# Kernel optimization log

Hardware: AMD Instinct MI355X
Metric: run time of the kernel (lower is better)

## Reference

```python
import jax, jax.numpy as jnp
import numpy as np

N, E, F, H, C, G = 100000, 1600000, 128, 128, 1, 512
NLAYERS, DT, ALPHA, GAMMA = 5, 1.0, 1.0, 1.0


def setup_inputs() -> dict:
    key = jax.random.key(0)
    ks = jax.random.split(key, 11)
    x = jax.random.normal(ks[0], (N, F), dtype=jnp.float32)
    edge_index = jax.random.randint(ks[1], (2, E), 0, N, dtype=jnp.int64)
    batch = jnp.sort(jax.random.randint(ks[2], (N,), 0, G, dtype=jnp.int64))
    s = 1.0 / np.sqrt(H).astype(np.float32)
    W_enc = jax.random.normal(ks[3], (H, F), jnp.float32) * (1.0 / np.sqrt(F))
    b_enc = jnp.zeros((H,), jnp.float32)
    W_conv = jax.random.normal(ks[4], (H, H), jnp.float32) * s
    b_conv = jnp.zeros((H,), jnp.float32)
    W_res = jax.random.normal(ks[5], (H, H), jnp.float32) * s
    b_res = jnp.zeros((H,), jnp.float32)
    W_dec = jax.random.normal(ks[6], (C, H), jnp.float32) * s
    b_dec = jnp.zeros((C,), jnp.float32)
    return {
        "x": x, "edge_index": edge_index, "batch": batch,
        "W_enc": W_enc, "b_enc": b_enc,
        "W_conv": W_conv, "b_conv": b_conv,
        "W_res": W_res, "b_res": b_res,
        "W_dec": W_dec, "b_dec": b_dec,
    }


def reference(x, edge_index, batch, W_enc, b_enc, W_conv, b_conv, W_res, b_res, W_dec, b_dec):
    src, dst = edge_index[0], edge_index[1]
    # GCN symmetric normalization with self-loops: deg = 1 + in-degree(dst)
    deg = jnp.zeros((N,), x.dtype).at[dst].add(1.0) + 1.0
    dinv = jax.lax.rsqrt(deg)
    norm = dinv[src] * dinv[dst]            # [E]
    self_norm = (dinv * dinv)[:, None]      # [N,1] self-loop coefficient

    def gcn_conv(X):
        xw = X @ W_conv.T                   # lin (bias=False)
        agg = jnp.zeros_like(xw).at[dst].add(norm[:, None] * xw[src])
        agg = agg + self_norm * xw          # self-loop term
        return agg + b_conv

    Y = x @ W_enc.T + b_enc
    Xs = Y
    for _ in range(NLAYERS):
        res = Xs @ W_res.T + b_res - Xs @ W_conv.T   # res(X) - conv.lin(X)
        Y = Y + DT * (jax.nn.relu(gcn_conv(Xs) + res) - ALPHA * Y - GAMMA * Xs)
        Xs = Xs + DT * Y
    out = Xs @ W_dec.T + b_dec               # [N, 1]
    pooled = jax.ops.segment_sum(out, batch, num_segments=G)  # [G, 1]
    return pooled.squeeze(-1)                # [G]
```

## Files before the change

### kernel.cpp

```cpp
#include <hip/hip_runtime.h>
#include <hip/hip_bf16.h>
#include <stdint.h>


#define HD 128
#define SCHUNK 2048

typedef __attribute__((ext_vector_type(4))) float f32x4;
typedef __attribute__((ext_vector_type(8))) float f32x8;
typedef __attribute__((ext_vector_type(8))) _Float16 f16x8;

__global__ __launch_bounds__(256) void k_deg(const int* __restrict__ dst, int E,
                                             int* __restrict__ cnt){
  int e = blockIdx.x * 256 + threadIdx.x;
  if (e < E) atomicAdd(&cnt[dst[e]], 1);
}

__global__ __launch_bounds__(256) void k_scan_part(const int* __restrict__ cnt,
                                                   int* __restrict__ bsum, int N){
  __shared__ int red[256];
  int t = threadIdx.x;
  int lo = blockIdx.x * SCHUNK + t * 8;
  int s = 0;
#pragma unroll
  for (int k = 0; k < 8; ++k){
    int i = lo + k;
    s += (i < N) ? cnt[i] : 0;
  }
  red[t] = s;
  __syncthreads();
  for (int off = 128; off > 0; off >>= 1){
    if (t < off) red[t] += red[t + off];
    __syncthreads();
  }
  if (t == 0) bsum[blockIdx.x] = red[0];
}

__global__ __launch_bounds__(1024) void k_scan_mid(const int* __restrict__ bsum,
                                                   int* __restrict__ boff, int nb,
                                                   int* __restrict__ rp, int N, int E){
  __shared__ int part[1024];
  int t = threadIdx.x;
  part[t] = (t < nb) ? bsum[t] : 0;
  __syncthreads();
  for (int off = 1; off < 1024; off <<= 1){
    int v = (t >= off) ? part[t - off] : 0;
    __syncthreads();
    part[t] += v;
    __syncthreads();
  }
  if (t < nb) boff[t] = (t == 0) ? 0 : part[t - 1];
  if (t == 0) rp[N] = E;
}

__global__ __launch_bounds__(256) void k_scan_apply(const int* __restrict__ cnt,
                                                    const int* __restrict__ boff,
                                                    int* __restrict__ rp,
                                                    float* __restrict__ dinv, int N){
  __shared__ int tsum[256];
  int t = threadIdx.x;
  int lo = blockIdx.x * SCHUNK + t * 8;
  int v[8];
  int s = 0;
#pragma unroll
  for (int k = 0; k < 8; ++k){
    int i = lo + k;
    v[k] = (i < N) ? cnt[i] : 0;
    s += v[k];
  }
  tsum[t] = s;
  __syncthreads();
  for (int off = 1; off < 256; off <<= 1){
    int u = (t >= off) ? tsum[t - off] : 0;
    __syncthreads();
    tsum[t] += u;
    __syncthreads();
  }
  int base = boff[blockIdx.x] + ((t == 0) ? 0 : tsum[t - 1]);
#pragma unroll
  for (int k = 0; k < 8; ++k){
    int i = lo + k;
    if (i < N){
      rp[i] = base;
      dinv[i] = rsqrtf((float)v[k] + 1.0f);
      base += v[k];
    }
  }
}

__global__ __launch_bounds__(256) void k_fill(const int* __restrict__ src,
                                              const int* __restrict__ dst, int E,
                                              const int* __restrict__ rp,
                                              int* cnt,
                                              const float* __restrict__ dinv,
                                              unsigned* __restrict__ col){
  int e = blockIdx.x * 256 + threadIdx.x;
  if (e >= E) return;
  int s = src[e], d = dst[e];
  int pos = rp[d] + atomicSub(&cnt[d], 1) - 1;
  float di = dinv[s];
  int deg1 = (int)(1.0f / (di * di) + 0.5f);
  col[pos] = ((unsigned)deg1 << 18) | (unsigned)s;
}

__global__ __launch_bounds__(256) void k_prep_w(const float* __restrict__ Wc,
                                                const float* __restrict__ Wr,
                                                const float* __restrict__ We,
                                                const float* __restrict__ bc,
                                                const float* __restrict__ br,
                                                _Float16* __restrict__ WcF,
                                                _Float16* __restrict__ WrF,
                                                _Float16* __restrict__ WeF,
                                                float* __restrict__ bias_sum){
  int i = blockIdx.x * 256 + threadIdx.x;
  if (i < HD * HD){
    WcF[i] = (_Float16)Wc[i];
    WrF[i] = (_Float16)Wr[i];
    WeF[i] = (_Float16)We[i];
  }
  if (i < HD) bias_sum[i] = bc[i] + br[i];
}

__global__ __launch_bounds__(256) void k_agg(const _Float16* __restrict__ XsH,
                                             const float* __restrict__ dinv,
                                             const int* __restrict__ rp,
                                             const unsigned* __restrict__ col,
                                             _Float16* __restrict__ U,
                                             int N){
  int w = threadIdx.x >> 6;
  int lane = threadIdx.x & 63;
  int q = lane >> 4;
  int ql = lane & 15;
  int node = blockIdx.x * 4 + w;
  if (node >= N) return;

  float acc[8];
#pragma unroll
  for (int i = 0; i < 8; ++i) acc[i] = 0.f;

  int b = rp[node], e = rp[node + 1];
  int j = b + q;
  for (; j + 12 < e; j += 16){
    unsigned r0 = col[j];
    unsigned r1 = col[j + 4];
    unsigned r2 = col[j + 8];
    unsigned r3 = col[j + 12];
    float w0 = rsqrtf((float)(r0 >> 18));
    float w1 = rsqrtf((float)(r1 >> 18));
    float w2 = rsqrtf((float)(r2 >> 18));
    float w3 = rsqrtf((float)(r3 >> 18));
    f16x8 v0 = ((const f16x8*)(XsH + (size_t)(r0 & 0x3FFFFu) * HD))[ql];
    f16x8 v1 = ((const f16x8*)(XsH + (size_t)(r1 & 0x3FFFFu) * HD))[ql];
    f16x8 v2 = ((const f16x8*)(XsH + (size_t)(r2 & 0x3FFFFu) * HD))[ql];
    f16x8 v3 = ((const f16x8*)(XsH + (size_t)(r3 & 0x3FFFFu) * HD))[ql];
#pragma unroll
    for (int i = 0; i < 8; ++i) acc[i] = fmaf(w0, (float)v0[i], acc[i]);
#pragma unroll
    for (int i = 0; i < 8; ++i) acc[i] = fmaf(w1, (float)v1[i], acc[i]);
#pragma unroll
    for (int i = 0; i < 8; ++i) acc[i] = fmaf(w2, (float)v2[i], acc[i]);
#pragma unroll
    for (int i = 0; i < 8; ++i) acc[i] = fmaf(w3, (float)v3[i], acc[i]);
  }
  for (; j < e; j += 4){
    unsigned r0 = col[j];
    float w0 = rsqrtf((float)(r0 >> 18));
    f16x8 v0 = ((const f16x8*)(XsH + (size_t)(r0 & 0x3FFFFu) * HD))[ql];
#pragma unroll
    for (int i = 0; i < 8; ++i) acc[i] = fmaf(w0, (float)v0[i], acc[i]);
  }

  float dn = dinv[node];
#pragma unroll
  for (int i = 0; i < 8; ++i){
    acc[i] += __shfl_xor(acc[i], 16, 64);
    acc[i] += __shfl_xor(acc[i], 32, 64);
    acc[i] *= dn;
  }
  if (q == 0){
    f16x8 o;
#pragma unroll
    for (int i = 0; i < 8; ++i) o[i] = (_Float16)acc[i];
    ((f16x8*)(U + (size_t)node * HD))[ql] = o;
  }
}

__global__ __launch_bounds__(256) void k_gemm(
    const float* __restrict__ A1f,
    const _Float16* __restrict__ A1h,
    const _Float16* A2h,
    const _Float16* __restrict__ W1,
    const _Float16* __restrict__ W2,
    const float* __restrict__ dinvp,
    const float* __restrict__ bias,
    _Float16* outXsH,
    const float* __restrict__ Wd, const float* __restrict__ bd,
    float* __restrict__ val,
    int N, int relu, int decode){
  __shared__ _Float16 wsm[HD * HD];
  f16x8* smv = (f16x8*)wsm;
  int t = threadIdx.x;

  {
    const f16x8* g1 = (const f16x8*)W1;
    for (int i = t; i < HD * HD / 8; i += 256){
      int row = i >> 4, slot = i & 15;
      smv[(row << 4) | (slot ^ (row & 7))] = g1[i];
    }
  }
  __syncthreads();

  int wid = blockIdx.x * 4 + (t >> 6);
  int row0 = wid * 32;
  bool act = (row0 < N);
  int rowb = act ? row0 : 0;
  int lane = t & 63;
  int r = lane & 15;
  int kg = lane >> 4;

  f32x4 acc[2][8];
#pragma unroll
  for (int s = 0; s < 2; ++s)
#pragma unroll
    for (int c = 0; c < 8; ++c) acc[s][c] = (f32x4)0.0f;

  const bool two = (A2h != nullptr);
  float sr[2] = {0.f, 0.f};
  if (two){
#pragma unroll
    for (int s = 0; s < 2; ++s){
      float d = dinvp[rowb + s * 16 + r];
      sr[s] = d * d - 1.0f;
    }
  }

#pragma unroll
  for (int kst = 0; kst < 4; ++kst){
    int k0 = kst * 32 + kg * 8;
    f16x8 a1[2];
#pragma unroll
    for (int s = 0; s < 2; ++s){
      size_t ao = (size_t)(rowb + s * 16 + r) * HD + k0;
      if (two){
        f16x8 uh = *(const f16x8*)(A1h + ao);
        f16x8 xv = *(const f16x8*)(A2h + ao);
#pragma unroll
        for (int i = 0; i < 8; ++i)
          a1[s][i] = (_Float16)fmaf(sr[s], (float)xv[i], (float)uh[i]);
      } else {
        f32x8 u = *(const f32x8*)(A1f + ao);
#pragma unroll
        for (int i = 0; i < 8; ++i) a1[s][i] = (_Float16)u[i];
      }
    }
    int swz = (kst * 4 + kg) ^ (r & 7);
#pragma unroll
    for (int ct = 0; ct < 8; ++ct){
      f16x8 b1 = smv[((ct * 16 + r) << 4) | swz];
#pragma unroll
      for (int s = 0; s < 2; ++s)
        acc[s][ct] = __builtin_amdgcn_mfma_f32_16x16x32_f16(a1[s], b1, acc[s][ct], 0, 0, 0);
    }
  }

  if (two){
    __syncthreads();
    const f16x8* g2 = (const f16x8*)W2;
    for (int i = t; i < HD * HD / 8; i += 256){
      int row = i >> 4, slot = i & 15;
      smv[(row << 4) | (slot ^ (row & 7))] = g2[i];
    }
    __syncthreads();
#pragma unroll
    for (int kst = 0; kst < 4; ++kst){
      int k0 = kst * 32 + kg * 8;
      f16x8 a2[2];
#pragma unroll
      for (int s = 0; s < 2; ++s){
        size_t ao = (size_t)(rowb + s * 16 + r) * HD + k0;
        a2[s] = *(const f16x8*)(A2h + ao);
      }
      int swz = (kst * 4 + kg) ^ (r & 7);
#pragma unroll
      for (int ct = 0; ct < 8; ++ct){
        f16x8 b2 = smv[((ct * 16 + r) << 4) | swz];
#pragma unroll
        for (int s = 0; s < 2; ++s)
          acc[s][ct] = __builtin_amdgcn_mfma_f32_16x16x32_f16(a2[s], b2, acc[s][ct], 0, 0, 0);
      }
    }
  }

  float rowp[2][4] = {{0.f,0.f,0.f,0.f},{0.f,0.f,0.f,0.f}};
#pragma unroll
  for (int s = 0; s < 2; ++s){
#pragma unroll
    for (int ct = 0; ct < 8; ++ct){
      int cc = ct * 16 + r;
      float bv = bias[cc];
      float wdv = decode ? Wd[cc] : 0.f;
#pragma unroll
      for (int j = 0; j < 4; ++j){
        float v = acc[s][ct][j] + bv;
        if (relu) v = fmaxf(v, 0.0f);
        if (decode){
          rowp[s][j] += v * wdv;
        } else if (act){
          int rr = row0 + s * 16 + kg * 4 + j;
          outXsH[(size_t)rr * HD + cc] = (_Float16)v;
        }
      }
    }
  }
  if (decode && act){
    float bd0 = bd[0];
#pragma unroll
    for (int s = 0; s < 2; ++s)
#pragma unroll
      for (int j = 0; j < 4; ++j){
        float tt = rowp[s][j];
        tt += __shfl_xor(tt, 1, 64);
        tt += __shfl_xor(tt, 2, 64);
        tt += __shfl_xor(tt, 4, 64);
        tt += __shfl_xor(tt, 8, 64);
        if (r == 0) val[row0 + s * 16 + kg * 4 + j] = tt + bd0;
      }
  }
}

#define POOL_CHUNK 1024
__global__ __launch_bounds__(256) void k_pool(const float* __restrict__ val,
                                              const int* __restrict__ batch,
                                              float* __restrict__ out, int N, int G){
  __shared__ float acc[4096];
  int t = threadIdx.x;
  int lo = blockIdx.x * POOL_CHUNK;
  int hi = min(lo + POOL_CHUNK, N);
  if (G <= 4096){
    for (int i = t; i < G; i += 256) acc[i] = 0.f;
    __syncthreads();
    for (int i = lo + t; i < hi; i += 256) atomicAdd(&acc[batch[i]], val[i]);
    __syncthreads();
    for (int i = t; i < G; i += 256){
      float v = acc[i];
      if (v != 0.f) atomicAdd(&out[i], v);
    }
  } else {
    for (int i = lo + t; i < hi; i += 256) atomicAdd(&out[batch[i]], val[i]);
  }
}

extern "C" void kernel_launch(void* const* d_in, const int* in_sizes, int n_in,
                              void* d_out, int out_size, void* d_ws, size_t ws_size,
                              hipStream_t stream){
  const float* x      = (const float*)d_in[0];
  const int*   ei     = (const int*)d_in[1];
  const int*   batch  = (const int*)d_in[2];
  const float* W_enc  = (const float*)d_in[3];
  const float* b_enc  = (const float*)d_in[4];
  const float* W_conv = (const float*)d_in[5];
  const float* b_conv = (const float*)d_in[6];
  const float* W_res  = (const float*)d_in[7];
  const float* b_res  = (const float*)d_in[8];
  const float* W_dec  = (const float*)d_in[9];
  const float* b_dec  = (const float*)d_in[10];

  const int N = in_sizes[0] / HD;
  const int E = in_sizes[1] / 2;
  float* out = (float*)d_out;

  char* ws = (char*)d_ws;
  size_t off = 0;
  auto alloc = [&](size_t bytes) -> char* {
    char* p = ws + off;
    off += (bytes + 255) & ~(size_t)255;
    return p;
  };
  int*   cnt   = (int*)  alloc((size_t)N * 4);
  int*   rp    = (int*)  alloc(((size_t)N + 1) * 4);
  float* dinv  = (float*)alloc((size_t)N * 4);
  int*   bsum  = (int*)  alloc(1024 * 4);
  int*   boff  = (int*)  alloc(1024 * 4);
  unsigned* col= (unsigned*)alloc((size_t)E * 4);
  _Float16* XsH= (_Float16*)alloc((size_t)N * HD * 2);
  _Float16* U  = (_Float16*)alloc((size_t)N * HD * 2);
  float* val   = (float*)alloc((size_t)N * 4);
  _Float16* WcF = (_Float16*)alloc((size_t)HD * HD * 2);
  _Float16* WrF = (_Float16*)alloc((size_t)HD * HD * 2);
  _Float16* WeF = (_Float16*)alloc((size_t)HD * HD * 2);
  float* bias_sum = (float*)alloc((size_t)HD * 4);

  hipMemsetAsync(cnt, 0, (size_t)N * 4, stream);
  hipMemsetAsync(out, 0, (size_t)out_size * 4, stream);

  const int* src = ei;
  const int* dst = ei + E;

  int nb = (N + SCHUNK - 1) / SCHUNK;

  k_deg       <<<(E + 255) / 256, 256, 0, stream>>>(dst, E, cnt);
  k_scan_part <<<nb, 256, 0, stream>>>(cnt, bsum, N);
  k_scan_mid  <<<1, 1024, 0, stream>>>(bsum, boff, nb, rp, N, E);
  k_scan_apply<<<nb, 256, 0, stream>>>(cnt, boff, rp, dinv, N);
  k_fill      <<<(E + 255) / 256, 256, 0, stream>>>(src, dst, E, rp, cnt, dinv, col);
  k_prep_w    <<<(HD * HD + 255) / 256, 256, 0, stream>>>(W_conv, W_res, W_enc, b_conv, b_res,
                                                          WcF, WrF, WeF, bias_sum);

  int gemm_blocks = ((N + 31) / 32 + 3) / 4;
  int node_blocks = (N + 3) / 4;

  k_gemm<<<gemm_blocks, 256, 0, stream>>>(x, nullptr, nullptr, WeF, nullptr,
                                          nullptr, b_enc, XsH,
                                          nullptr, nullptr, nullptr, N, 0, 0);

  for (int l = 0; l < 5; ++l){
    k_agg<<<node_blocks, 256, 0, stream>>>(XsH, dinv, rp, col, U, N);
    int last = (l == 4);
    k_gemm<<<gemm_blocks, 256, 0, stream>>>(nullptr, U, XsH, WcF, WrF,
                                            dinv, bias_sum, XsH,
                                            W_dec, b_dec, val, N, 1, last);
  }

  k_pool<<<(N + POOL_CHUNK - 1) / POOL_CHUNK, 256, 0, stream>>>(val, batch, out, N, out_size);
}
```

Baseline: 648.8 us.

## Fuse neighbor aggregation into the per-layer GEMM kernel via LDS staging

Merges the separate aggregation kernel and the layer GEMM into a single k_layer kernel. Each block gathers neighbor features for its 128 nodes into a swizzled LDS tile, then runs the MFMA GEMM straight from LDS. This removes the global write and re-read of the intermediate U buffer and one launch per layer. Because the kernel now reads and writes different node rows, it ping-pongs between two feature buffers. The costs are 64KB of LDS per block, which lowers occupancy and latency hiding for the gather, and fewer, larger blocks with some load imbalance from varying degrees.

```diff
diff --git a/kernel.cpp b/kernel.cpp
--- a/kernel.cpp
+++ b/kernel.cpp
@@ -121,86 +121,15 @@
   if (i < HD) bias_sum[i] = bc[i] + br[i];
 }
 
-__global__ __launch_bounds__(256) void k_agg(const _Float16* __restrict__ XsH,
-                                             const float* __restrict__ dinv,
-                                             const int* __restrict__ rp,
-                                             const unsigned* __restrict__ col,
-                                             _Float16* __restrict__ U,
-                                             int N){
-  int w = threadIdx.x >> 6;
-  int lane = threadIdx.x & 63;
-  int q = lane >> 4;
-  int ql = lane & 15;
-  int node = blockIdx.x * 4 + w;
-  if (node >= N) return;
-
-  float acc[8];
-#pragma unroll
-  for (int i = 0; i < 8; ++i) acc[i] = 0.f;
-
-  int b = rp[node], e = rp[node + 1];
-  int j = b + q;
-  for (; j + 12 < e; j += 16){
-    unsigned r0 = col[j];
-    unsigned r1 = col[j + 4];
-    unsigned r2 = col[j + 8];
-    unsigned r3 = col[j + 12];
-    float w0 = rsqrtf((float)(r0 >> 18));
-    float w1 = rsqrtf((float)(r1 >> 18));
-    float w2 = rsqrtf((float)(r2 >> 18));
-    float w3 = rsqrtf((float)(r3 >> 18));
-    f16x8 v0 = ((const f16x8*)(XsH + (size_t)(r0 & 0x3FFFFu) * HD))[ql];
-    f16x8 v1 = ((const f16x8*)(XsH + (size_t)(r1 & 0x3FFFFu) * HD))[ql];
-    f16x8 v2 = ((const f16x8*)(XsH + (size_t)(r2 & 0x3FFFFu) * HD))[ql];
-    f16x8 v3 = ((const f16x8*)(XsH + (size_t)(r3 & 0x3FFFFu) * HD))[ql];
-#pragma unroll
-    for (int i = 0; i < 8; ++i) acc[i] = fmaf(w0, (float)v0[i], acc[i]);
-#pragma unroll
-    for (int i = 0; i < 8; ++i) acc[i] = fmaf(w1, (float)v1[i], acc[i]);
-#pragma unroll
-    for (int i = 0; i < 8; ++i) acc[i] = fmaf(w2, (float)v2[i], acc[i]);
-#pragma unroll
-    for (int i = 0; i < 8; ++i) acc[i] = fmaf(w3, (float)v3[i], acc[i]);
-  }
-  for (; j < e; j += 4){
-    unsigned r0 = col[j];
-    float w0 = rsqrtf((float)(r0 >> 18));
-    f16x8 v0 = ((const f16x8*)(XsH + (size_t)(r0 & 0x3FFFFu) * HD))[ql];
-#pragma unroll
-    for (int i = 0; i < 8; ++i) acc[i] = fmaf(w0, (float)v0[i], acc[i]);
-  }
-
-  float dn = dinv[node];
-#pragma unroll
-  for (int i = 0; i < 8; ++i){
-    acc[i] += __shfl_xor(acc[i], 16, 64);
-    acc[i] += __shfl_xor(acc[i], 32, 64);
-    acc[i] *= dn;
-  }
-  if (q == 0){
-    f16x8 o;
-#pragma unroll
-    for (int i = 0; i < 8; ++i) o[i] = (_Float16)acc[i];
-    ((f16x8*)(U + (size_t)node * HD))[ql] = o;
-  }
-}
-
-__global__ __launch_bounds__(256) void k_gemm(
+__global__ __launch_bounds__(256) void k_enc(
     const float* __restrict__ A1f,
-    const _Float16* __restrict__ A1h,
-    const _Float16* A2h,
     const _Float16* __restrict__ W1,
-    const _Float16* __restrict__ W2,
-    const float* __restrict__ dinvp,
     const float* __restrict__ bias,
-    _Float16* outXsH,
-    const float* __restrict__ Wd, const float* __restrict__ bd,
-    float* __restrict__ val,
-    int N, int relu, int decode){
+    _Float16* __restrict__ outXsH,
+    int N){
   __shared__ _Float16 wsm[HD * HD];
   f16x8* smv = (f16x8*)wsm;
   int t = threadIdx.x;
-
   {
     const f16x8* g1 = (const f16x8*)W1;
     for (int i = t; i < HD * HD / 8; i += 256){
@@ -224,34 +153,15 @@
 #pragma unroll
     for (int c = 0; c < 8; ++c) acc[s][c] = (f32x4)0.0f;
 
-  const bool two = (A2h != nullptr);
-  float sr[2] = {0.f, 0.f};
-  if (two){
-#pragma unroll
-    for (int s = 0; s < 2; ++s){
-      float d = dinvp[rowb + s * 16 + r];
-      sr[s] = d * d - 1.0f;
-    }
-  }
-
 #pragma unroll
   for (int kst = 0; kst < 4; ++kst){
     int k0 = kst * 32 + kg * 8;
     f16x8 a1[2];
 #pragma unroll
     for (int s = 0; s < 2; ++s){
-      size_t ao = (size_t)(rowb + s * 16 + r) * HD + k0;
-      if (two){
-        f16x8 uh = *(const f16x8*)(A1h + ao);
-        f16x8 xv = *(const f16x8*)(A2h + ao);
-#pragma unroll
-        for (int i = 0; i < 8; ++i)
-          a1[s][i] = (_Float16)fmaf(sr[s], (float)xv[i], (float)uh[i]);
-      } else {
-        f32x8 u = *(const f32x8*)(A1f + ao);
-#pragma unroll
-        for (int i = 0; i < 8; ++i) a1[s][i] = (_Float16)u[i];
-      }
+      f32x8 u = *(const f32x8*)(A1f + (size_t)(rowb + s * 16 + r) * HD + k0);
+#pragma unroll
+      for (int i = 0; i < 8; ++i) a1[s][i] = (_Float16)u[i];
     }
     int swz = (kst * 4 + kg) ^ (r & 7);
 #pragma unroll
@@ -262,32 +172,175 @@
         acc[s][ct] = __builtin_amdgcn_mfma_f32_16x16x32_f16(a1[s], b1, acc[s][ct], 0, 0, 0);
     }
   }
-
-  if (two){
-    __syncthreads();
+  if (act){
+#pragma unroll
+    for (int s = 0; s < 2; ++s)
+#pragma unroll
+      for (int ct = 0; ct < 8; ++ct){
+        int cc = ct * 16 + r;
+        float bv = bias[cc];
+#pragma unroll
+        for (int j = 0; j < 4; ++j){
+          int rr = row0 + s * 16 + kg * 4 + j;
+          outXsH[(size_t)rr * HD + cc] = (_Float16)(acc[s][ct][j] + bv);
+        }
+      }
+  }
+}
+
+__global__ __launch_bounds__(256) void k_layer(
+    const _Float16* __restrict__ Xp,
+    const float* __restrict__ dinv,
+    const int* __restrict__ rp,
+    const unsigned* __restrict__ col,
+    const _Float16* __restrict__ W1,
+    const _Float16* __restrict__ W2,
+    const float* __restrict__ bias,
+    _Float16* __restrict__ Xn,
+    const float* __restrict__ Wd, const float* __restrict__ bd,
+    float* __restrict__ val,
+    int N, int decode){
+  __shared__ _Float16 usm[HD * HD];
+  __shared__ _Float16 wsm[HD * HD];
+  f16x8* uv  = (f16x8*)usm;
+  f16x8* smv = (f16x8*)wsm;
+  int t = threadIdx.x;
+
+  {
+    const f16x8* g1 = (const f16x8*)W1;
+    for (int i = t; i < HD * HD / 8; i += 256){
+      int row = i >> 4, slot = i & 15;
+      smv[(row << 4) | (slot ^ (row & 7))] = g1[i];
+    }
+  }
+
+  int wv = t >> 6;
+  int lane = t & 63;
+  int q = lane >> 4;
+  int ql = lane & 15;
+  int blk0 = (int)blockIdx.x * 128;
+
+  for (int k = 0; k < 32; ++k){
+    int ln = wv * 32 + k;
+    int node = blk0 + ln;
+    float acc[8];
+#pragma unroll
+    for (int i = 0; i < 8; ++i) acc[i] = 0.f;
+    if (node < N){
+      int b = rp[node], e = rp[node + 1];
+      int j = b + q;
+      for (; j + 12 < e; j += 16){
+        unsigned r0 = col[j];
+        unsigned r1 = col[j + 4];
+        unsigned r2 = col[j + 8];
+        unsigned r3 = col[j + 12];
+        float w0 = rsqrtf((float)(r0 >> 18));
+        float w1 = rsqrtf((float)(r1 >> 18));
+        float w2 = rsqrtf((float)(r2 >> 18));
+        float w3 = rsqrtf((float)(r3 >> 18));
+        f16x8 v0 = ((const f16x8*)(Xp + (size_t)(r0 & 0x3FFFFu) * HD))[ql];
+        f16x8 v1 = ((const f16x8*)(Xp + (size_t)(r1 & 0x3FFFFu) * HD))[ql];
+        f16x8 v2 = ((const f16x8*)(Xp + (size_t)(r2 & 0x3FFFFu) * HD))[ql];
+        f16x8 v3 = ((const f16x8*)(Xp + (size_t)(r3 & 0x3FFFFu) * HD))[ql];
+#pragma unroll
+        for (int i = 0; i < 8; ++i) acc[i] = fmaf(w0, (float)v0[i], acc[i]);
+#pragma unroll
+        for (int i = 0; i < 8; ++i) acc[i] = fmaf(w1, (float)v1[i], acc[i]);
+#pragma unroll
+        for (int i = 0; i < 8; ++i) acc[i] = fmaf(w2, (float)v2[i], acc[i]);
+#pragma unroll
+        for (int i = 0; i < 8; ++i) acc[i] = fmaf(w3, (float)v3[i], acc[i]);
+      }
+      for (; j < e; j += 4){
+        unsigned r0 = col[j];
+        float w0 = rsqrtf((float)(r0 >> 18));
+        f16x8 v0 = ((const f16x8*)(Xp + (size_t)(r0 & 0x3FFFFu) * HD))[ql];
+#pragma unroll
+        for (int i = 0; i < 8; ++i) acc[i] = fmaf(w0, (float)v0[i], acc[i]);
+      }
+      float dn = dinv[node];
+#pragma unroll
+      for (int i = 0; i < 8; ++i){
+        acc[i] += __shfl_xor(acc[i], 16, 64);
+        acc[i] += __shfl_xor(acc[i], 32, 64);
+        acc[i] *= dn;
+      }
+    }
+    if (q == 0){
+      f16x8 o;
+#pragma unroll
+      for (int i = 0; i < 8; ++i) o[i] = (_Float16)acc[i];
+      uv[(ln << 4) | (ql ^ (ln & 7))] = o;
+    }
+  }
+  __syncthreads();
+
+  int row0 = blk0 + wv * 32;
+  bool act = (row0 < N);
+  int rowb = act ? row0 : 0;
+  int r = lane & 15;
+  int kg = lane >> 4;
+
+  f32x4 acc2[2][8];
+#pragma unroll
+  for (int s = 0; s < 2; ++s)
+#pragma unroll
+    for (int c = 0; c < 8; ++c) acc2[s][c] = (f32x4)0.0f;
+
+  float sr[2];
+#pragma unroll
+  for (int s = 0; s < 2; ++s){
+    float d = dinv[rowb + s * 16 + r];
+    sr[s] = d * d - 1.0f;
+  }
+
+#pragma unroll
+  for (int kst = 0; kst < 4; ++kst){
+    int k0 = kst * 32 + kg * 8;
+    int swz = (kst * 4 + kg) ^ (r & 7);
+    f16x8 a1[2];
+#pragma unroll
+    for (int s = 0; s < 2; ++s){
+      int lrow = wv * 32 + s * 16 + r;
+      f16x8 uh = uv[(lrow << 4) | swz];
+      f16x8 xv = *(const f16x8*)(Xp + (size_t)(rowb + s * 16 + r) * HD + k0);
+#pragma unroll
+      for (int i = 0; i < 8; ++i)
+        a1[s][i] = (_Float16)fmaf(sr[s], (float)xv[i], (float)uh[i]);
+    }
+#pragma unroll
+    for (int ct = 0; ct < 8; ++ct){
+      f16x8 b1 = smv[((ct * 16 + r) << 4) | swz];
+#pragma unroll
+      for (int s = 0; s < 2; ++s)
+        acc2[s][ct] = __builtin_amdgcn_mfma_f32_16x16x32_f16(a1[s], b1, acc2[s][ct], 0, 0, 0);
+    }
+  }
+
+  __syncthreads();
+  {
     const f16x8* g2 = (const f16x8*)W2;
     for (int i = t; i < HD * HD / 8; i += 256){
       int row = i >> 4, slot = i & 15;
       smv[(row << 4) | (slot ^ (row & 7))] = g2[i];
     }
-    __syncthreads();
-#pragma unroll
-    for (int kst = 0; kst < 4; ++kst){
-      int k0 = kst * 32 + kg * 8;
-      f16x8 a2[2];
-#pragma unroll
-      for (int s = 0; s < 2; ++s){
-        size_t ao = (size_t)(rowb + s * 16 + r) * HD + k0;
-        a2[s] = *(const f16x8*)(A2h + ao);
-      }
-      int swz = (kst * 4 + kg) ^ (r & 7);
-#pragma unroll
-      for (int ct = 0; ct < 8; ++ct){
-        f16x8 b2 = smv[((ct * 16 + r) << 4) | swz];
-#pragma unroll
-        for (int s = 0; s < 2; ++s)
-          acc[s][ct] = __builtin_amdgcn_mfma_f32_16x16x32_f16(a2[s], b2, acc[s][ct], 0, 0, 0);
-      }
+  }
+  __syncthreads();
+
+#pragma unroll
+  for (int kst = 0; kst < 4; ++kst){
+    int k0 = kst * 32 + kg * 8;
+    int swz = (kst * 4 + kg) ^ (r & 7);
+    f16x8 a2[2];
+#pragma unroll
+    for (int s = 0; s < 2; ++s)
+      a2[s] = *(const f16x8*)(Xp + (size_t)(rowb + s * 16 + r) * HD + k0);
+#pragma unroll
+    for (int ct = 0; ct < 8; ++ct){
+      f16x8 b2 = smv[((ct * 16 + r) << 4) | swz];
+#pragma unroll
+      for (int s = 0; s < 2; ++s)
+        acc2[s][ct] = __builtin_amdgcn_mfma_f32_16x16x32_f16(a2[s], b2, acc2[s][ct], 0, 0, 0);
     }
   }
 
@@ -301,13 +354,12 @@
       float wdv = decode ? Wd[cc] : 0.f;
 #pragma unroll
       for (int j = 0; j < 4; ++j){
-        float v = acc[s][ct][j] + bv;
-        if (relu) v = fmaxf(v, 0.0f);
+        float v = fmaxf(acc2[s][ct][j] + bv, 0.0f);
         if (decode){
           rowp[s][j] += v * wdv;
         } else if (act){
           int rr = row0 + s * 16 + kg * 4 + j;
-          outXsH[(size_t)rr * HD + cc] = (_Float16)v;
+          Xn[(size_t)rr * HD + cc] = (_Float16)v;
         }
       }
     }
@@ -382,8 +434,8 @@
   int*   bsum  = (int*)  alloc(1024 * 4);
   int*   boff  = (int*)  alloc(1024 * 4);
   unsigned* col= (unsigned*)alloc((size_t)E * 4);
-  _Float16* XsH= (_Float16*)alloc((size_t)N * HD * 2);
-  _Float16* U  = (_Float16*)alloc((size_t)N * HD * 2);
+  _Float16* XsA= (_Float16*)alloc((size_t)N * HD * 2);
+  _Float16* XsB= (_Float16*)alloc((size_t)N * HD * 2);
   float* val   = (float*)alloc((size_t)N * 4);
   _Float16* WcF = (_Float16*)alloc((size_t)HD * HD * 2);
   _Float16* WrF = (_Float16*)alloc((size_t)HD * HD * 2);
@@ -406,19 +458,21 @@
   k_prep_w    <<<(HD * HD + 255) / 256, 256, 0, stream>>>(W_conv, W_res, W_enc, b_conv, b_res,
                                                           WcF, WrF, WeF, bias_sum);
 
-  int gemm_blocks = ((N + 31) / 32 + 3) / 4;
-  int node_blocks = (N + 3) / 4;
-
-  k_gemm<<<gemm_blocks, 256, 0, stream>>>(x, nullptr, nullptr, WeF, nullptr,
-                                          nullptr, b_enc, XsH,
-                                          nullptr, nullptr, nullptr, N, 0, 0);
-
+  int enc_blocks = ((N + 31) / 32 + 3) / 4;
+  int layer_blocks = (N + 127) / 128;
+
+  k_enc<<<enc_blocks, 256, 0, stream>>>(x, WeF, b_enc, XsA, N);
+
+  const _Float16* cur = XsA;
+  _Float16* nxt = XsB;
   for (int l = 0; l < 5; ++l){
-    k_agg<<<node_blocks, 256, 0, stream>>>(XsH, dinv, rp, col, U, N);
     int last = (l == 4);
-    k_gemm<<<gemm_blocks, 256, 0, stream>>>(nullptr, U, XsH, WcF, WrF,
-                                            dinv, bias_sum, XsH,
-                                            W_dec, b_dec, val, N, 1, last);
+    k_layer<<<layer_blocks, 256, 0, stream>>>(cur, dinv, rp, col, WcF, WrF,
+                                              bias_sum, nxt,
+                                              W_dec, b_dec, val, N, last);
+    const _Float16* tmp = nxt;
+    nxt = (_Float16*)cur;
+    cur = tmp;
   }
 
   k_pool<<<(N + POOL_CHUNK - 1) / POOL_CHUNK, 256, 0, stream>>>(val, batch, out, N, out_size);
```

Measured after the change: 1.112 ms. 1.71x slower.
